# Performance work log

Measured on AMD Instinct MI355X. Metric: run time of the kernel, lower is better.

The kernel has to match this reference:

```python
import jax, jax.numpy as jnp
import numpy as np

EMB = 512
HID = 512
NCLASS = 50257
BATCH = 64
STEPS = 256


def setup_inputs() -> dict:
    key = jax.random.key(0)
    ks = jax.random.split(key, 14)
    s_e = 1.0 / np.sqrt(EMB)
    s_h = 1.0 / np.sqrt(HID)
    inp = {
        "X": jax.random.randint(ks[0], (BATCH, STEPS), 0, NCLASS, dtype=jnp.int32),
        "emb": jax.random.normal(ks[1], (NCLASS, EMB), jnp.float32) * 0.02,
        # layer 1: gates concatenated in order [i, f, g, o]
        "Wi": jax.random.normal(ks[2], (EMB, 4 * HID), jnp.float32) * s_e,
        "Wh": jax.random.normal(ks[3], (HID, 4 * HID), jnp.float32) * s_h,
        "bi": jax.random.normal(ks[4], (4 * HID,), jnp.float32) * 0.01,
        "bh": jax.random.normal(ks[5], (4 * HID,), jnp.float32) * 0.01,
        # layer 2 (computed but unused for the output, as in the original)
        "Wi1": jax.random.normal(ks[6], (HID, 4 * HID), jnp.float32) * s_h,
        "Wh1": jax.random.normal(ks[7], (HID, 4 * HID), jnp.float32) * s_h,
        "bi1": jax.random.normal(ks[8], (4 * HID,), jnp.float32) * 0.01,
        "bh1": jax.random.normal(ks[9], (4 * HID,), jnp.float32) * 0.01,
        # output projection (nn.Linear(n_hidden, n_class, bias=False) => W: [n_class, n_hidden])
        "Wout": jax.random.normal(ks[10], (NCLASS, HID), jnp.float32) * s_h,
        "bout": jnp.ones((NCLASS,), jnp.float32),
    }
    return inp


def _gates(pre):
    i, f, g, o = jnp.split(pre, 4, axis=-1)
    return jax.nn.sigmoid(i), jax.nn.sigmoid(f), jnp.tanh(g), jax.nn.sigmoid(o)


def reference(X, emb, Wi, Wh, bi, bh, Wi1, Wh1, bi1, bh1, Wout, bout):
    x = emb[X]  # [B, T, E]
    B = x.shape[0]
    # precompute input projections for layer 1 for all timesteps: [T, B, 4H]
    xw = jnp.einsum("bte,eh->tbh", x, Wi) + bi + bh

    h0 = jnp.zeros((B, HID), x.dtype)
    carry0 = (h0, h0, h0, h0)  # h, c, h1, c1

    def step(carry, xw_t):
        h, c, h1, c1 = carry
        i, f, g, o = _gates(xw_t + h @ Wh)
        c = f * c + i * g
        h = o * jnp.tanh(c)
        i1, f1, g1, o1 = _gates(h @ Wi1 + bi1 + h1 @ Wh1 + bh1)
        c1 = f1 * c1 + i1 * g1
        h1 = o1 * jnp.tanh(c1)
        return (h, c, h1, c1), None

    (h, c, h1, c1), _ = jax.lax.scan(step, carry0, xw)
    # original: outputs[-1] is layer-1 h at the last timestep
    return h @ Wout.T + bout
```

## Files before the change

### kernel.cpp

```cpp
#include <hip/hip_runtime.h>
#include <cstdint>
#include <cstddef>

#define EMB    512
#define HID    512
#define NCLASS 50257
#define BATCH  64
#define STEPS  256
#define FOURH  2048
#define NBLK   64

typedef __attribute__((ext_vector_type(8))) short    bf16x8;
typedef __attribute__((ext_vector_type(4))) float    f32x4;
typedef __attribute__((ext_vector_type(8))) _Float16 h8v;

__device__ __forceinline__ unsigned short f2bf(float f) {
    union { float f; unsigned int u; } v; v.f = f;
    unsigned int u = v.u;
    return (unsigned short)((u + 0x7fffu + ((u >> 16) & 1u)) >> 16);
}


__global__ void k_bias(const float* __restrict__ bi, const float* __restrict__ bh,
                       float* __restrict__ bias) {
    int i = blockIdx.x * 256 + threadIdx.x;
    if (i < FOURH) bias[i] = bi[i] + bh[i];
}

__global__ void k_wit(const float* __restrict__ Wi, unsigned short* __restrict__ WiT) {
    int n = blockIdx.x;
    int l = threadIdx.x;
    int k0 = l * 8;
    unsigned short t[8];
#pragma unroll
    for (int i = 0; i < 8; i++)
        t[i] = f2bf(Wi[(size_t)(k0 + i) * FOURH + n]);
    uint4 v;
    v.x = (unsigned)t[0] | ((unsigned)t[1] << 16);
    v.y = (unsigned)t[2] | ((unsigned)t[3] << 16);
    v.z = (unsigned)t[4] | ((unsigned)t[5] << 16);
    v.w = (unsigned)t[6] | ((unsigned)t[7] << 16);
    *(uint4*)(WiT + (size_t)n * EMB + k0) = v;
}

__global__ void k_whP(const float* __restrict__ Wh, _Float16* __restrict__ WhP) {
    int idx = blockIdx.x;
    int bidb = idx >> 5, c = idx & 31;
    int ul   = ((c >> 4) << 2) + ((c >> 2) & 3);
    int gate = c & 3;
    int gcol = gate * 512 + bidb * 8 + ul;
    int k0 = threadIdx.x * 8;
    h8v r;
#pragma unroll
    for (int i = 0; i < 8; i++)
        r[i] = (_Float16)Wh[(size_t)(k0 + i) * FOURH + gcol];
    *(h8v*)(WhP + (size_t)idx * 512 + k0) = r;
}

__global__ void k_gather(const int* __restrict__ X, const float* __restrict__ emb,
                         unsigned short* __restrict__ XA) {
    int chunk = blockIdx.x * 256 + threadIdx.x;
    int m  = chunk >> 6;
    int c8 = (chunk & 63) * 8;
    int t = m >> 6, b = m & 63;
    int row = X[b * STEPS + t];
    const float4* src = (const float4*)(emb + (size_t)row * EMB + c8);
    float4 f0 = src[0], f1 = src[1];
    uint4 v;
    v.x = (unsigned)f2bf(f0.x) | ((unsigned)f2bf(f0.y) << 16);
    v.y = (unsigned)f2bf(f0.z) | ((unsigned)f2bf(f0.w) << 16);
    v.z = (unsigned)f2bf(f1.x) | ((unsigned)f2bf(f1.y) << 16);
    v.w = (unsigned)f2bf(f1.z) | ((unsigned)f2bf(f1.w) << 16);
    *(uint4*)(XA + (size_t)m * EMB + c8) = v;
}

__global__ void k_zero(int* __restrict__ p, int n) {
    int i = blockIdx.x * 256 + threadIdx.x;
    if (i < n) p[i] = 0;
}

__global__ __launch_bounds__(256) void k_gemm1(const unsigned short* __restrict__ XA,
                                               const unsigned short* __restrict__ WiT,
                                               const float* __restrict__ bias,
                                               float* __restrict__ XWT) {
    __shared__ unsigned short Al[64 * 48];
    __shared__ unsigned short Bl[64 * 48];
    const int t  = blockIdx.y;
    const int m0 = t * 64;
    const int n0 = blockIdx.x * 64;
    const int tid  = threadIdx.x;
    const int w    = tid >> 6;
    const int lane = tid & 63;
    const int quad = lane >> 4;
    const int l16  = lane & 15;
    const int ar = tid >> 2;
    const int ac = (tid & 3) * 8;

    f32x4 acc[4];
#pragma unroll
    for (int i = 0; i < 4; i++) acc[i] = (f32x4){0.f, 0.f, 0.f, 0.f};

    for (int kk = 0; kk < 16; kk++) {
        const int k0 = kk * 32;
        __syncthreads();
        *(uint4*)(&Al[ar * 48 + ac]) = *(const uint4*)(XA  + (size_t)(m0 + ar) * EMB + k0 + ac);
        *(uint4*)(&Bl[ar * 48 + ac]) = *(const uint4*)(WiT + (size_t)(n0 + ar) * EMB + k0 + ac);
        __syncthreads();
        bf16x8 afrag = *(const bf16x8*)(&Bl[(w * 16 + l16) * 48 + quad * 8]);
#pragma unroll
        for (int mt = 0; mt < 4; mt++) {
            bf16x8 bfrag = *(const bf16x8*)(&Al[(mt * 16 + l16) * 48 + quad * 8]);
            acc[mt] = __builtin_amdgcn_mfma_f32_16x16x32_bf16(afrag, bfrag, acc[mt], 0, 0, 0);
        }
    }
    float bv[4];
#pragma unroll
    for (int r = 0; r < 4; r++) bv[r] = bias[n0 + w * 16 + quad * 4 + r];
#pragma unroll
    for (int mt = 0; mt < 4; mt++)
#pragma unroll
        for (int r = 0; r < 4; r++)
            XWT[((size_t)t * FOURH + n0 + w * 16 + quad * 4 + r) * 64 + mt * 16 + l16]
                = acc[mt][r] + bv[r];
}

__global__ __launch_bounds__(256, 1) void k_rnn(const float* __restrict__ XWT,
                                                const _Float16* __restrict__ WhP,
                                                _Float16* __restrict__ hG,
                                                float* __restrict__ hfinal,
                                                unsigned int* __restrict__ flags) {
    __shared__ _Float16 hw[64 * 8];
    __shared__ unsigned wcnt;
    __shared__ int      ep;

    const int tid  = threadIdx.x;
    const int bid  = blockIdx.x;
    const int lane = tid & 63;
    const int bt   = tid >> 6;
    const int quad = lane >> 4;
    const int l16  = lane & 15;
    const int b    = bt * 16 + l16;

    if (tid == 0) { wcnt = 0; ep = 0; }
    __syncthreads();

    h8v afrag[2][16];
#pragma unroll
    for (int tt = 0; tt < 2; tt++) {
        const _Float16* wsrc = WhP + ((size_t)(bid * 32 + tt * 16 + l16)) * 512 + quad * 8;
#pragma unroll
        for (int kk = 0; kk < 16; kk++) afrag[tt][kk] = *(const h8v*)(wsrc + kk * 32);
    }

    float c0 = 0.f, c1 = 0.f;
    const size_t xwo0 = (size_t)(bid * 8 + quad) * 64 + b;
    const size_t xwo1 = (size_t)(bid * 8 + 4 + quad) * 64 + b;

    float xwA[4], xwB[4];
#pragma unroll
    for (int g = 0; g < 4; g++) {
        xwA[g] = XWT[(size_t)g * 32768 + xwo0];
        xwB[g] = XWT[(size_t)g * 32768 + xwo1];
    }

    for (int t = 0; t < STEPS; t++) {
        if (t > 0) {
            if (bt == 0) {
                const unsigned tgt = (unsigned)t;
                unsigned guard = 0;
                unsigned v = __hip_atomic_load(&flags[lane * 16],
                                               __ATOMIC_RELAXED, __HIP_MEMORY_SCOPE_AGENT);
                while (!__all(v >= tgt)) {
                    __builtin_amdgcn_s_sleep(1);
                    if (++guard > (1u << 17)) break;
                    v = __hip_atomic_load(&flags[lane * 16],
                                          __ATOMIC_RELAXED, __HIP_MEMORY_SCOPE_AGENT);
                }
                if (lane == 0) *(volatile int*)&ep = t;
            } else {
                unsigned guard = 0;
                while (*(volatile int*)&ep < t) {
                    __builtin_amdgcn_s_sleep(1);
                    if (++guard > (1u << 20)) break;
                }
            }
        }

        const char* hsrc = (const char*)hG + (size_t)(t & 1) * 65536
                         + (size_t)b * 1024 + quad * 16;
        uint4 qv[16];
#pragma unroll
        for (int kk = 0; kk < 16; kk++)
            asm volatile("global_load_dwordx4 %0, %1, off sc0 sc1"
                         : "=v"(qv[kk]) : "v"(hsrc + kk * 64));
        asm volatile("s_waitcnt vmcnt(0)" ::: "memory");
        __builtin_amdgcn_sched_barrier(0);

        f32x4 aA0 = {0.f,0.f,0.f,0.f}, aA1 = {0.f,0.f,0.f,0.f};
        f32x4 aB0 = {0.f,0.f,0.f,0.f}, aB1 = {0.f,0.f,0.f,0.f};
#pragma unroll
        for (int kk = 0; kk < 16; kk += 2) {
            union { uint4 q; h8v v; } f0, f1;
            f0.q = qv[kk]; f1.q = qv[kk + 1];
            aA0 = __builtin_amdgcn_mfma_f32_16x16x32_f16(afrag[0][kk],     f0.v, aA0, 0, 0, 0);
            aB0 = __builtin_amdgcn_mfma_f32_16x16x32_f16(afrag[1][kk],     f0.v, aB0, 0, 0, 0);
            aA1 = __builtin_amdgcn_mfma_f32_16x16x32_f16(afrag[0][kk + 1], f1.v, aA1, 0, 0, 0);
            aB1 = __builtin_amdgcn_mfma_f32_16x16x32_f16(afrag[1][kk + 1], f1.v, aB1, 0, 0, 0);
        }
        f32x4 accA = aA0 + aA1;
        f32x4 accB = aB0 + aB1;

        float iA = 1.f / (1.f + __expf(-(accA[0] + xwA[0])));
        float fA = 1.f / (1.f + __expf(-(accA[1] + xwA[1])));
        float gA = tanhf(accA[2] + xwA[2]);
        float oA = 1.f / (1.f + __expf(-(accA[3] + xwA[3])));
        c0 = fA * c0 + iA * gA;
        float hnA = oA * tanhf(c0);

        float iB = 1.f / (1.f + __expf(-(accB[0] + xwB[0])));
        float fB = 1.f / (1.f + __expf(-(accB[1] + xwB[1])));
        float gB = tanhf(accB[2] + xwB[2]);
        float oB = 1.f / (1.f + __expf(-(accB[3] + xwB[3])));
        c1 = fB * c1 + iB * gB;
        float hnB = oB * tanhf(c1);

        if (t == STEPS - 1) {
            hfinal[(size_t)b * HID + bid * 8 + quad]     = hnA;
            hfinal[(size_t)b * HID + bid * 8 + 4 + quad] = hnB;
            break;
        }

        hw[b * 8 + quad]     = (_Float16)hnA;
        hw[b * 8 + 4 + quad] = (_Float16)hnB;
        asm volatile("s_waitcnt lgkmcnt(0)" ::: "memory");
        if (quad == 0) {
            const unsigned long long* src = (const unsigned long long*)(hw + b * 8);
            unsigned long long lo = src[0], hi = src[1];
            unsigned long long* dst = (unsigned long long*)((char*)hG
                + (size_t)((t + 1) & 1) * 65536 + (size_t)b * 1024 + bid * 16);
            __hip_atomic_store(dst,     lo, __ATOMIC_RELAXED, __HIP_MEMORY_SCOPE_AGENT);
            __hip_atomic_store(dst + 1, hi, __ATOMIC_RELAXED, __HIP_MEMORY_SCOPE_AGENT);
        }
        asm volatile("s_waitcnt vmcnt(0)" ::: "memory");
        if (lane == 0) {
            unsigned old = atomicAdd(&wcnt, 1u);
            if (old == (unsigned)(4 * t + 3))
                __hip_atomic_store(&flags[bid * 16], (unsigned)(t + 1),
                                   __ATOMIC_RELAXED, __HIP_MEMORY_SCOPE_AGENT);
        }

        {
            const float* xp = XWT + (size_t)(t + 1) * (FOURH * 64);
#pragma unroll
            for (int g = 0; g < 4; g++) {
                xwA[g] = xp[(size_t)g * 32768 + xwo0];
                xwB[g] = xp[(size_t)g * 32768 + xwo1];
            }
            asm volatile("" :: "v"(xwA[0]), "v"(xwA[1]), "v"(xwA[2]), "v"(xwA[3]),
                              "v"(xwB[0]), "v"(xwB[1]), "v"(xwB[2]), "v"(xwB[3]));
        }
    }
}

__global__ __launch_bounds__(128) void k_out(const float* __restrict__ Wout,
                                             const float* __restrict__ bout,
                                             const float* __restrict__ hfinal,
                                             float* __restrict__ out) {
    __shared__ float hl[BATCH * 128];
    const int tid = threadIdx.x;
    const int n = blockIdx.x * 128 + tid;
    const bool valid = n < NCLASS;
    float acc[BATCH];
#pragma unroll
    for (int b = 0; b < BATCH; b++) acc[b] = 0.f;
    const float4* W4 = (const float4*)Wout;
    const float4* h4 = (const float4*)hfinal;
    float4* hl4 = (float4*)hl;

    for (int kq = 0; kq < 4; kq++) {
        __syncthreads();
#pragma unroll
        for (int i = 0; i < 16; i++) {
            int f = i * 128 + tid;
            int b = f >> 5, kk = f & 31;
            hl4[f] = h4[b * 128 + kq * 32 + kk];
        }
        __syncthreads();
        if (valid) {
            for (int kk = 0; kk < 32; kk++) {
                float4 wv = W4[(size_t)n * 128 + kq * 32 + kk];
#pragma unroll
                for (int b = 0; b < BATCH; b++) {
                    float4 hv = hl4[b * 32 + kk];
                    acc[b] = fmaf(wv.x, hv.x, acc[b]);
                    acc[b] = fmaf(wv.y, hv.y, acc[b]);
                    acc[b] = fmaf(wv.z, hv.z, acc[b]);
                    acc[b] = fmaf(wv.w, hv.w, acc[b]);
                }
            }
        }
    }
    if (valid) {
        float bv = bout[n];
        for (int b = 0; b < BATCH; b++)
            out[(size_t)b * NCLASS + n] = acc[b] + bv;
    }
}


extern "C" void kernel_launch(void* const* d_in, const int* in_sizes, int n_in,
                              void* d_out, int out_size, void* d_ws, size_t ws_size,
                              hipStream_t stream) {
    const int*   X    = (const int*)  d_in[0];
    const float* emb  = (const float*)d_in[1];
    const float* Wi   = (const float*)d_in[2];
    const float* Wh   = (const float*)d_in[3];
    const float* bi   = (const float*)d_in[4];
    const float* bh   = (const float*)d_in[5];
    const float* Wout = (const float*)d_in[10];
    const float* bout = (const float*)d_in[11];
    float* out = (float*)d_out;

    char* w = (char*)d_ws;
    float*          XWT    = (float*)(w);
    unsigned short* XA     = (unsigned short*)(w + 134217728);
    _Float16*       hG     = (_Float16*)(w + 150732800);
    unsigned int*   flags  = (unsigned int*)(w + 150863872);
    unsigned short* WiT    = (unsigned short*)(w + 150994944);
    _Float16*       WhP    = (_Float16*)(w + 153092096);
    float*          bias   = (float*)(w + 155189248);
    float*          hfinal = (float*)(w + 155197440);

    k_bias  <<<8,    256, 0, stream>>>(bi, bh, bias);
    k_wit   <<<2048,  64, 0, stream>>>(Wi, WiT);
    k_whP   <<<2048,  64, 0, stream>>>(Wh, WhP);
    k_gather<<<4096, 256, 0, stream>>>(X, emb, XA);
    k_gemm1 <<<dim3(32, 256), 256, 0, stream>>>(XA, WiT, bias, XWT);
    k_zero  <<<132,  256, 0, stream>>>((int*)hG, 33792);

    k_rnn   <<<NBLK, 256, 0, stream>>>(XWT, WhP, hG, hfinal, flags);

    k_out   <<<393,  128, 0, stream>>>(Wout, bout, hfinal, out);
}
```

Before: 1.641 ms.

## Publish per-wavefront step flags and store packed h pairs directly

The hidden-state write-back no longer goes through shared memory. Each lane packs its two fp16 outputs into one 32-bit store, and the recurrent weight packing permutes the K index so those interleaved positions line up with the MFMA operand order. The per-block LDS atomic counter that gated the block flag is replaced by one flag per wavefront, and pollers read four flags at once with a single dwordx4 load. This removes an LDS round trip and the atomic serialisation from the per-step critical path, at the cost of four times as many flags to poll.

```diff
diff --git a/kernel.cpp b/kernel.cpp
--- a/kernel.cpp
+++ b/kernel.cpp
@@ -52,8 +52,11 @@
     int k0 = threadIdx.x * 8;
     h8v r;
 #pragma unroll
-    for (int i = 0; i < 8; i++)
-        r[i] = (_Float16)Wh[(size_t)(k0 + i) * FOURH + gcol];
+    for (int i = 0; i < 8; i++) {
+        int K  = k0 + i;
+        int nu = (K & ~7) + ((K >> 1) & 3) + ((K & 1) << 2);
+        r[i] = (_Float16)Wh[(size_t)nu * FOURH + gcol];
+    }
     *(h8v*)(WhP + (size_t)idx * 512 + k0) = r;
 }
 
@@ -129,9 +132,7 @@
                                                 _Float16* __restrict__ hG,
                                                 float* __restrict__ hfinal,
                                                 unsigned int* __restrict__ flags) {
-    __shared__ _Float16 hw[64 * 8];
-    __shared__ unsigned wcnt;
-    __shared__ int      ep;
+    __shared__ int ep;
 
     const int tid  = threadIdx.x;
     const int bid  = blockIdx.x;
@@ -141,7 +142,7 @@
     const int l16  = lane & 15;
     const int b    = bt * 16 + l16;
 
-    if (tid == 0) { wcnt = 0; ep = 0; }
+    if (tid == 0) ep = 0;
     __syncthreads();
 
     h8v afrag[2][16];
@@ -167,14 +168,17 @@
         if (t > 0) {
             if (bt == 0) {
                 const unsigned tgt = (unsigned)t;
+                const char* fp = (const char*)(flags + lane * 16);
                 unsigned guard = 0;
-                unsigned v = __hip_atomic_load(&flags[lane * 16],
-                                               __ATOMIC_RELAXED, __HIP_MEMORY_SCOPE_AGENT);
-                while (!__all(v >= tgt)) {
+                while (true) {
+                    uint4 f;
+                    asm volatile("global_load_dwordx4 %0, %1, off sc0 sc1"
+                                 : "=v"(f) : "v"(fp));
+                    asm volatile("s_waitcnt vmcnt(0)" ::: "memory");
+                    bool ok = (f.x >= tgt) & (f.y >= tgt) & (f.z >= tgt) & (f.w >= tgt);
+                    if (__all(ok)) break;
                     __builtin_amdgcn_s_sleep(1);
                     if (++guard > (1u << 17)) break;
-                    v = __hip_atomic_load(&flags[lane * 16],
-                                          __ATOMIC_RELAXED, __HIP_MEMORY_SCOPE_AGENT);
                 }
                 if (lane == 0) *(volatile int*)&ep = t;
             } else {
@@ -230,24 +234,18 @@
             break;
         }
 
-        hw[b * 8 + quad]     = (_Float16)hnA;
-        hw[b * 8 + 4 + quad] = (_Float16)hnB;
-        asm volatile("s_waitcnt lgkmcnt(0)" ::: "memory");
-        if (quad == 0) {
-            const unsigned long long* src = (const unsigned long long*)(hw + b * 8);
-            unsigned long long lo = src[0], hi = src[1];
-            unsigned long long* dst = (unsigned long long*)((char*)hG
-                + (size_t)((t + 1) & 1) * 65536 + (size_t)b * 1024 + bid * 16);
-            __hip_atomic_store(dst,     lo, __ATOMIC_RELAXED, __HIP_MEMORY_SCOPE_AGENT);
-            __hip_atomic_store(dst + 1, hi, __ATOMIC_RELAXED, __HIP_MEMORY_SCOPE_AGENT);
+        {
+            union { _Float16 h[2]; unsigned u; } pk;
+            pk.h[0] = (_Float16)hnA;
+            pk.h[1] = (_Float16)hnB;
+            unsigned* dst = (unsigned*)((char*)hG + (size_t)((t + 1) & 1) * 65536
+                          + (size_t)b * 1024 + bid * 16 + quad * 4);
+            __hip_atomic_store(dst, pk.u, __ATOMIC_RELAXED, __HIP_MEMORY_SCOPE_AGENT);
         }
         asm volatile("s_waitcnt vmcnt(0)" ::: "memory");
-        if (lane == 0) {
-            unsigned old = atomicAdd(&wcnt, 1u);
-            if (old == (unsigned)(4 * t + 3))
-                __hip_atomic_store(&flags[bid * 16], (unsigned)(t + 1),
-                                   __ATOMIC_RELAXED, __HIP_MEMORY_SCOPE_AGENT);
-        }
+        if (lane == 0)
+            __hip_atomic_store(&flags[bid * 16 + bt], (unsigned)(t + 1),
+                               __ATOMIC_RELAXED, __HIP_MEMORY_SCOPE_AGENT);
 
         {
             const float* xp = XWT + (size_t)(t + 1) * (FOURH * 64);
```

New measurement: 1.688 ms. +2.9%, slower.
